# Optimization experiments

Hardware: AMD Instinct MI355X
Metric: run time of the kernel (lower is better)

## Reference

```python
import jax, jax.numpy as jnp
import numpy as np

BETA = 0.25
NUM_EMB = 50
EMB_DIM = 192


def setup_inputs() -> dict:
    key = jax.random.key(0)
    k1, k2 = jax.random.split(key)
    N = 262144
    inputs = jax.random.normal(k1, (N, EMB_DIM), dtype=jnp.float32)
    # nn.Embedding init: uniform(-1/num_embeddings, 1/num_embeddings)
    embed_w = jax.random.uniform(k2, (NUM_EMB, EMB_DIM), dtype=jnp.float32,
                                 minval=-1.0 / NUM_EMB, maxval=1.0 / NUM_EMB)
    return {"inputs": inputs, "embed_w": embed_w}


def reference(inputs, embed_w):
    # flat_input: [N, D] (inputs already flattened to last-dim = embedding_dim)
    flat = inputs.reshape(-1, EMB_DIM)
    distances = (jnp.sum(flat * flat, axis=1, keepdims=True)
                 + jnp.sum(embed_w * embed_w, axis=1)
                 - 2.0 * (flat @ embed_w.T))
    encoding_indices = jnp.argmin(distances, axis=1)[:, None]  # [N, 1]
    # one-hot scatter + matmul in the original == direct gather of nearest code
    quantized = embed_w[encoding_indices[:, 0]]  # [N, D]
    sg = jax.lax.stop_gradient
    commitloss = (jnp.mean((sg(quantized) - flat) ** 2)
                  + BETA * jnp.mean((quantized - sg(flat)) ** 2))
    # straight-through estimator
    quantized_st = flat + sg(quantized - flat)
    contrastloss = jnp.float32(0.0)
    return (quantized_st, encoding_indices, commitloss, contrastloss)
```

## Files before the change

### kernel.cpp

```cpp
#include <hip/hip_runtime.h>
#include <cfloat>

#define NUM_EMB 50
#define EMB_DIM 192
#define ESTRIDE 196

__device__ __forceinline__ float np_tree8(const float r[8]) {
#pragma clang fp contract(off)
    return ((r[0] + r[1]) + (r[2] + r[3])) + ((r[4] + r[5]) + (r[6] + r[7]));
}

__device__ float np_sumsq_192(const float* __restrict__ p) {
#pragma clang fp contract(off)
    float tot[2];
#pragma unroll
    for (int h = 0; h < 2; ++h) {
        float r[8];
#pragma unroll
        for (int l = 0; l < 8; ++l) r[l] = 0.f;
        const float* q = p + h * 96;
        for (int t = 0; t < 12; ++t)
#pragma unroll
            for (int l = 0; l < 8; ++l) {
                float v = q[t * 8 + l];
                float pr = v * v;
                r[l] = r[l] + pr;
            }
        tot[h] = np_tree8(r);
    }
    return tot[0] + tot[1];
}

__global__ __launch_bounds__(256, 4) void vq_fused(
    const float* __restrict__ x, const float* __restrict__ ew,
    float* __restrict__ out_q, float* __restrict__ out_idx,
    float* __restrict__ out_loss, int N)
{
    __shared__ __align__(16) float sE[NUM_EMB * ESTRIDE];
    __shared__ float sB[NUM_EMB];

    for (int i = threadIdx.x; i < NUM_EMB * EMB_DIM; i += blockDim.x) {
        int k = i / EMB_DIM, j = i - k * EMB_DIM;
        sE[k * ESTRIDE + j] = ew[i];
    }
    __syncthreads();
    if (threadIdx.x < NUM_EMB)
        sB[threadIdx.x] = np_sumsq_192(&sE[threadIdx.x * ESTRIDE]);
    __syncthreads();

    const int row = blockIdx.x * blockDim.x + threadIdx.x;
    const float4* xr = (const float4*)(x + (size_t)row * EMB_DIM);

    float acc[NUM_EMB];
#pragma unroll
    for (int k = 0; k < NUM_EMB; ++k) acc[k] = 0.f;

    float rA[8];
    float aHalf[2];

    for (int m = 0; m < 6; ++m) {
        float4 f4[8];
#pragma unroll
        for (int q = 0; q < 8; ++q) f4[q] = xr[m * 8 + q];

        if ((m % 3) == 0) {
#pragma unroll
            for (int l = 0; l < 8; ++l) rA[l] = 0.f;
        }
        {
#pragma clang fp contract(off)
#pragma unroll
            for (int q = 0; q < 8; ++q) {
                float p0 = f4[q].x * f4[q].x; rA[(q * 4 + 0) & 7] = rA[(q * 4 + 0) & 7] + p0;
                float p1 = f4[q].y * f4[q].y; rA[(q * 4 + 1) & 7] = rA[(q * 4 + 1) & 7] + p1;
                float p2 = f4[q].z * f4[q].z; rA[(q * 4 + 2) & 7] = rA[(q * 4 + 2) & 7] + p2;
                float p3 = f4[q].w * f4[q].w; rA[(q * 4 + 3) & 7] = rA[(q * 4 + 3) & 7] + p3;
            }
        }
        if ((m % 3) == 2) aHalf[m / 3] = np_tree8(rA);

        const float* eb = ew + m * 32;
#pragma unroll
        for (int k = 0; k < NUM_EMB; ++k) {
            const float* ek = eb + k * EMB_DIM;
            float4 e4[8];
#pragma unroll
            for (int q = 0; q < 8; ++q) e4[q] = *(const float4*)&ek[q * 4];
#pragma unroll
            for (int q = 0; q < 8; ++q) {
                acc[k] = __builtin_fmaf(f4[q].x, e4[q].x, acc[k]);
                acc[k] = __builtin_fmaf(f4[q].y, e4[q].y, acc[k]);
                acc[k] = __builtin_fmaf(f4[q].z, e4[q].z, acc[k]);
                acc[k] = __builtin_fmaf(f4[q].w, e4[q].w, acc[k]);
            }
        }
    }

    float best; int bidx;
    {
#pragma clang fp contract(off)
        float a = aHalf[0] + aHalf[1];
        best = FLT_MAX; bidx = 0;
#pragma unroll
        for (int k = 0; k < NUM_EMB; ++k) {
            float t1 = a + sB[k];
            float u  = 2.0f * acc[k];
            float d  = t1 - u;
            if (d < best) { best = d; bidx = k; }
        }
    }
    out_idx[row] = (float)bidx;

    float contrib = best;
#pragma unroll
    for (int off = 1; off < 64; off <<= 1) contrib += __shfl_xor(contrib, off);
    if ((threadIdx.x & 63) == 0) atomicAdd(out_loss, contrib);

    {
        const int lane = threadIdx.x & 63;
        const int c = lane & 7;
        const int rr = lane >> 3;
        const int waveRow0 = row & ~63;
#pragma unroll
        for (int g = 0; g < 8; ++g) {
            const int kk = __shfl(bidx, g * 8 + rr);
            const int wrow = waveRow0 + g * 8 + rr;
            float4* qrow = (float4*)(out_q + (size_t)wrow * EMB_DIM);
            const float* erow = &sE[kk * ESTRIDE];
#pragma unroll
            for (int t = 0; t < 6; ++t)
                qrow[c + 8 * t] = *(const float4*)&erow[(c + 8 * t) * 4];
        }
    }
}

__global__ void vq_init(float* out_loss) { out_loss[0] = 0.f; out_loss[1] = 0.f; }

__global__ void vq_finalize(float* __restrict__ out_loss, int N)
{
    double mean = (double)out_loss[0] / ((double)N * (double)EMB_DIM);
    out_loss[0] = (float)(1.25 * mean);
    out_loss[1] = 0.f;
}

extern "C" void kernel_launch(void* const* d_in, const int* in_sizes, int n_in,
                              void* d_out, int out_size, void* d_ws, size_t ws_size,
                              hipStream_t stream)
{
    const float* x  = (const float*)d_in[0];
    const float* ew = (const float*)d_in[1];
    const int N = in_sizes[0] / EMB_DIM;

    float* out_q    = (float*)d_out;
    float* out_idx  = out_q + (size_t)N * EMB_DIM;
    float* out_loss = out_idx + N;

    vq_init<<<1, 1, 0, stream>>>(out_loss);
    vq_fused<<<N / 256, 256, 0, stream>>>(x, ew, out_q, out_idx, out_loss, N);
    vq_finalize<<<1, 1, 0, stream>>>(out_loss, N);
}
```

Before: 420.1 us.

## Hold full input row in registers and stream codebook pairs with running argmin

Each thread now loads its whole 192-float input row into registers once, then loops over codebook entries two at a time, computing full dot products and updating the argmin as it goes. The 50-entry accumulator array goes away. Launch bounds are relaxed from 4 to 2 blocks per SM to give room for the larger register footprint. This trades per-codebook accumulators for a register-resident row. It reorders the FMA accumulation per code, which could change rounding relative to the staged version, and it lowers occupancy.

```diff
diff --git a/kernel.cpp b/kernel.cpp
--- a/kernel.cpp
+++ b/kernel.cpp
@@ -31,7 +31,7 @@
     return tot[0] + tot[1];
 }
 
-__global__ __launch_bounds__(256, 4) void vq_fused(
+__global__ __launch_bounds__(256, 2) void vq_fused(
     const float* __restrict__ x, const float* __restrict__ ew,
     float* __restrict__ out_q, float* __restrict__ out_idx,
     float* __restrict__ out_loss, int N)
@@ -49,64 +49,69 @@
     __syncthreads();
 
     const int row = blockIdx.x * blockDim.x + threadIdx.x;
-    const float4* xr = (const float4*)(x + (size_t)row * EMB_DIM);
+    const float4* xg = (const float4*)(x + (size_t)row * EMB_DIM);
 
-    float acc[NUM_EMB];
+    float4 xr[48];
 #pragma unroll
-    for (int k = 0; k < NUM_EMB; ++k) acc[k] = 0.f;
+    for (int q = 0; q < 48; ++q) xr[q] = xg[q];
 
-    float rA[8];
-    float aHalf[2];
+    float a;
+    {
+#pragma clang fp contract(off)
+        float tot[2];
+#pragma unroll
+        for (int h = 0; h < 2; ++h) {
+            float r[8];
+#pragma unroll
+            for (int l = 0; l < 8; ++l) r[l] = 0.f;
+#pragma unroll
+            for (int t = 0; t < 12; ++t) {
+                const float4 va = xr[h * 24 + t * 2];
+                const float4 vb = xr[h * 24 + t * 2 + 1];
+                float p0 = va.x * va.x; r[0] = r[0] + p0;
+                float p1 = va.y * va.y; r[1] = r[1] + p1;
+                float p2 = va.z * va.z; r[2] = r[2] + p2;
+                float p3 = va.w * va.w; r[3] = r[3] + p3;
+                float p4 = vb.x * vb.x; r[4] = r[4] + p4;
+                float p5 = vb.y * vb.y; r[5] = r[5] + p5;
+                float p6 = vb.z * vb.z; r[6] = r[6] + p6;
+                float p7 = vb.w * vb.w; r[7] = r[7] + p7;
+            }
+            tot[h] = np_tree8(r);
+        }
+        a = tot[0] + tot[1];
+    }
 
-    for (int m = 0; m < 6; ++m) {
-        float4 f4[8];
+    float best = FLT_MAX; int bidx = 0;
+    for (int kp = 0; kp < NUM_EMB / 2; ++kp) {
+        const float* e0 = ew + (size_t)(2 * kp) * EMB_DIM;
+        const float* e1 = e0 + EMB_DIM;
+        float a0 = 0.f, a1 = 0.f;
 #pragma unroll
-        for (int q = 0; q < 8; ++q) f4[q] = xr[m * 8 + q];
-
-        if ((m % 3) == 0) {
-#pragma unroll
-            for (int l = 0; l < 8; ++l) rA[l] = 0.f;
+        for (int q = 0; q < 48; ++q) {
+            const float4 ea = *(const float4*)&e0[q * 4];
+            const float4 eb = *(const float4*)&e1[q * 4];
+            const float4 xv = xr[q];
+            a0 = __builtin_fmaf(xv.x, ea.x, a0);
+            a0 = __builtin_fmaf(xv.y, ea.y, a0);
+            a0 = __builtin_fmaf(xv.z, ea.z, a0);
+            a0 = __builtin_fmaf(xv.w, ea.w, a0);
+            a1 = __builtin_fmaf(xv.x, eb.x, a1);
+            a1 = __builtin_fmaf(xv.y, eb.y, a1);
+            a1 = __builtin_fmaf(xv.z, eb.z, a1);
+            a1 = __builtin_fmaf(xv.w, eb.w, a1);
         }
         {
 #pragma clang fp contract(off)
-#pragma unroll
-            for (int q = 0; q < 8; ++q) {
-                float p0 = f4[q].x * f4[q].x; rA[(q * 4 + 0) & 7] = rA[(q * 4 + 0) & 7] + p0;
-                float p1 = f4[q].y * f4[q].y; rA[(q * 4 + 1) & 7] = rA[(q * 4 + 1) & 7] + p1;
-                float p2 = f4[q].z * f4[q].z; rA[(q * 4 + 2) & 7] = rA[(q * 4 + 2) & 7] + p2;
-                float p3 = f4[q].w * f4[q].w; rA[(q * 4 + 3) & 7] = rA[(q * 4 + 3) & 7] + p3;
-            }
-        }
-        if ((m % 3) == 2) aHalf[m / 3] = np_tree8(rA);
-
-        const float* eb = ew + m * 32;
-#pragma unroll
-        for (int k = 0; k < NUM_EMB; ++k) {
-            const float* ek = eb + k * EMB_DIM;
-            float4 e4[8];
-#pragma unroll
-            for (int q = 0; q < 8; ++q) e4[q] = *(const float4*)&ek[q * 4];
-#pragma unroll
-            for (int q = 0; q < 8; ++q) {
-                acc[k] = __builtin_fmaf(f4[q].x, e4[q].x, acc[k]);
-                acc[k] = __builtin_fmaf(f4[q].y, e4[q].y, acc[k]);
-                acc[k] = __builtin_fmaf(f4[q].z, e4[q].z, acc[k]);
-                acc[k] = __builtin_fmaf(f4[q].w, e4[q].w, acc[k]);
-            }
-        }
-    }
-
-    float best; int bidx;
-    {
-#pragma clang fp contract(off)
-        float a = aHalf[0] + aHalf[1];
-        best = FLT_MAX; bidx = 0;
-#pragma unroll
-        for (int k = 0; k < NUM_EMB; ++k) {
-            float t1 = a + sB[k];
-            float u  = 2.0f * acc[k];
-            float d  = t1 - u;
-            if (d < best) { best = d; bidx = k; }
+            const float sb0 = sB[2 * kp], sb1 = sB[2 * kp + 1];
+            float t0 = a + sb0;
+            float u0 = 2.0f * a0;
+            float d0 = t0 - u0;
+            if (d0 < best) { best = d0; bidx = 2 * kp; }
+            float t1 = a + sb1;
+            float u1 = 2.0f * a1;
+            float d1 = t1 - u1;
+            if (d1 < best) { best = d1; bidx = 2 * kp + 1; }
         }
     }
     out_idx[row] = (float)bidx;
```

Measured after the change: 520.3 us. 1.24x slower.

## Process two rows per thread and read codebook from shared memory

Applied to the files above, without the earlier changes.

Each thread now computes distances for two input rows (r0 and r0+N/2), so every codebook element loaded feeds two FMA chains. The codebook loads switch from global memory to the padded LDS copy. The grid is halved and launch bounds are relaxed to 2 blocks per SM to make room for the doubled accumulator registers. The cost is higher register pressure and lower occupancy, and the m-loop is no longer unrolled.

```diff
diff --git a/kernel.cpp b/kernel.cpp
--- a/kernel.cpp
+++ b/kernel.cpp
@@ -31,7 +31,7 @@
     return tot[0] + tot[1];
 }
 
-__global__ __launch_bounds__(256, 4) void vq_fused(
+__global__ __launch_bounds__(256, 2) void vq_fused(
     const float* __restrict__ x, const float* __restrict__ ew,
     float* __restrict__ out_q, float* __restrict__ out_idx,
     float* __restrict__ out_loss, int N)
@@ -48,70 +48,102 @@
         sB[threadIdx.x] = np_sumsq_192(&sE[threadIdx.x * ESTRIDE]);
     __syncthreads();
 
-    const int row = blockIdx.x * blockDim.x + threadIdx.x;
-    const float4* xr = (const float4*)(x + (size_t)row * EMB_DIM);
-
-    float acc[NUM_EMB];
-#pragma unroll
-    for (int k = 0; k < NUM_EMB; ++k) acc[k] = 0.f;
-
-    float rA[8];
-    float aHalf[2];
-
+    const int r0 = blockIdx.x * blockDim.x + threadIdx.x;
+    const int half = N >> 1;
+    const float4* xg0 = (const float4*)(x + (size_t)r0 * EMB_DIM);
+    const float4* xg1 = (const float4*)(x + (size_t)(r0 + half) * EMB_DIM);
+
+    float acc0[NUM_EMB], acc1[NUM_EMB];
+#pragma unroll
+    for (int k = 0; k < NUM_EMB; ++k) { acc0[k] = 0.f; acc1[k] = 0.f; }
+
+    float rA0[8], rA1[8];
+    float aHalf0[2], aHalf1[2];
+
+#pragma unroll 1
     for (int m = 0; m < 6; ++m) {
-        float4 f4[8];
-#pragma unroll
-        for (int q = 0; q < 8; ++q) f4[q] = xr[m * 8 + q];
+        float4 fa[8], fb[8];
+#pragma unroll
+        for (int q = 0; q < 8; ++q) fa[q] = xg0[m * 8 + q];
+#pragma unroll
+        for (int q = 0; q < 8; ++q) fb[q] = xg1[m * 8 + q];
+#pragma unroll
+        for (int q = 0; q < 8; ++q)
+            asm volatile("" : "+v"(fa[q].x), "+v"(fa[q].y), "+v"(fa[q].z), "+v"(fa[q].w));
+#pragma unroll
+        for (int q = 0; q < 8; ++q)
+            asm volatile("" : "+v"(fb[q].x), "+v"(fb[q].y), "+v"(fb[q].z), "+v"(fb[q].w));
 
         if ((m % 3) == 0) {
 #pragma unroll
-            for (int l = 0; l < 8; ++l) rA[l] = 0.f;
+            for (int l = 0; l < 8; ++l) { rA0[l] = 0.f; rA1[l] = 0.f; }
         }
         {
 #pragma clang fp contract(off)
 #pragma unroll
             for (int q = 0; q < 8; ++q) {
-                float p0 = f4[q].x * f4[q].x; rA[(q * 4 + 0) & 7] = rA[(q * 4 + 0) & 7] + p0;
-                float p1 = f4[q].y * f4[q].y; rA[(q * 4 + 1) & 7] = rA[(q * 4 + 1) & 7] + p1;
-                float p2 = f4[q].z * f4[q].z; rA[(q * 4 + 2) & 7] = rA[(q * 4 + 2) & 7] + p2;
-                float p3 = f4[q].w * f4[q].w; rA[(q * 4 + 3) & 7] = rA[(q * 4 + 3) & 7] + p3;
-            }
-        }
-        if ((m % 3) == 2) aHalf[m / 3] = np_tree8(rA);
-
-        const float* eb = ew + m * 32;
+                float p0 = fa[q].x * fa[q].x; rA0[(q * 4 + 0) & 7] = rA0[(q * 4 + 0) & 7] + p0;
+                float p1 = fa[q].y * fa[q].y; rA0[(q * 4 + 1) & 7] = rA0[(q * 4 + 1) & 7] + p1;
+                float p2 = fa[q].z * fa[q].z; rA0[(q * 4 + 2) & 7] = rA0[(q * 4 + 2) & 7] + p2;
+                float p3 = fa[q].w * fa[q].w; rA0[(q * 4 + 3) & 7] = rA0[(q * 4 + 3) & 7] + p3;
+            }
+#pragma unroll
+            for (int q = 0; q < 8; ++q) {
+                float p0 = fb[q].x * fb[q].x; rA1[(q * 4 + 0) & 7] = rA1[(q * 4 + 0) & 7] + p0;
+                float p1 = fb[q].y * fb[q].y; rA1[(q * 4 + 1) & 7] = rA1[(q * 4 + 1) & 7] + p1;
+                float p2 = fb[q].z * fb[q].z; rA1[(q * 4 + 2) & 7] = rA1[(q * 4 + 2) & 7] + p2;
+                float p3 = fb[q].w * fb[q].w; rA1[(q * 4 + 3) & 7] = rA1[(q * 4 + 3) & 7] + p3;
+            }
+        }
+        if ((m % 3) == 2) { aHalf0[m / 3] = np_tree8(rA0); aHalf1[m / 3] = np_tree8(rA1); }
+
 #pragma unroll
         for (int k = 0; k < NUM_EMB; ++k) {
-            const float* ek = eb + k * EMB_DIM;
+            const float* ek = &sE[k * ESTRIDE + m * 32];
             float4 e4[8];
 #pragma unroll
-            for (int q = 0; q < 8; ++q) e4[q] = *(const float4*)&ek[q * 4];
-#pragma unroll
-            for (int q = 0; q < 8; ++q) {
-                acc[k] = __builtin_fmaf(f4[q].x, e4[q].x, acc[k]);
-                acc[k] = __builtin_fmaf(f4[q].y, e4[q].y, acc[k]);
-                acc[k] = __builtin_fmaf(f4[q].z, e4[q].z, acc[k]);
-                acc[k] = __builtin_fmaf(f4[q].w, e4[q].w, acc[k]);
-            }
-        }
-    }
-
-    float best; int bidx;
+            for (int h = 0; h < 8; ++h) e4[h] = *(const float4*)&ek[h * 4];
+#pragma unroll
+            for (int h = 0; h < 8; ++h) {
+                acc0[k] = __builtin_fmaf(fa[h].x, e4[h].x, acc0[k]);
+                acc0[k] = __builtin_fmaf(fa[h].y, e4[h].y, acc0[k]);
+                acc0[k] = __builtin_fmaf(fa[h].z, e4[h].z, acc0[k]);
+                acc0[k] = __builtin_fmaf(fa[h].w, e4[h].w, acc0[k]);
+            }
+#pragma unroll
+            for (int h = 0; h < 8; ++h) {
+                acc1[k] = __builtin_fmaf(fb[h].x, e4[h].x, acc1[k]);
+                acc1[k] = __builtin_fmaf(fb[h].y, e4[h].y, acc1[k]);
+                acc1[k] = __builtin_fmaf(fb[h].z, e4[h].z, acc1[k]);
+                acc1[k] = __builtin_fmaf(fb[h].w, e4[h].w, acc1[k]);
+            }
+        }
+    }
+
+    float best0, best1; int bidx0, bidx1;
     {
 #pragma clang fp contract(off)
-        float a = aHalf[0] + aHalf[1];
-        best = FLT_MAX; bidx = 0;
+        float a0 = aHalf0[0] + aHalf0[1];
+        float a1 = aHalf1[0] + aHalf1[1];
+        best0 = FLT_MAX; bidx0 = 0;
+        best1 = FLT_MAX; bidx1 = 0;
 #pragma unroll
         for (int k = 0; k < NUM_EMB; ++k) {
-            float t1 = a + sB[k];
-            float u  = 2.0f * acc[k];
-            float d  = t1 - u;
-            if (d < best) { best = d; bidx = k; }
-        }
-    }
-    out_idx[row] = (float)bidx;
-
-    float contrib = best;
+            float sb = sB[k];
+            float t0 = a0 + sb;
+            float u0 = 2.0f * acc0[k];
+            float d0 = t0 - u0;
+            if (d0 < best0) { best0 = d0; bidx0 = k; }
+            float t1 = a1 + sb;
+            float u1 = 2.0f * acc1[k];
+            float d1 = t1 - u1;
+            if (d1 < best1) { best1 = d1; bidx1 = k; }
+        }
+    }
+    out_idx[r0] = (float)bidx0;
+    out_idx[r0 + half] = (float)bidx1;
+
+    float contrib = best0 + best1;
 #pragma unroll
     for (int off = 1; off < 64; off <<= 1) contrib += __shfl_xor(contrib, off);
     if ((threadIdx.x & 63) == 0) atomicAdd(out_loss, contrib);
@@ -120,11 +152,21 @@
         const int lane = threadIdx.x & 63;
         const int c = lane & 7;
         const int rr = lane >> 3;
-        const int waveRow0 = row & ~63;
+        const int waveRow0 = r0 & ~63;
 #pragma unroll
         for (int g = 0; g < 8; ++g) {
-            const int kk = __shfl(bidx, g * 8 + rr);
+            const int kk = __shfl(bidx0, g * 8 + rr);
             const int wrow = waveRow0 + g * 8 + rr;
+            float4* qrow = (float4*)(out_q + (size_t)wrow * EMB_DIM);
+            const float* erow = &sE[kk * ESTRIDE];
+#pragma unroll
+            for (int t = 0; t < 6; ++t)
+                qrow[c + 8 * t] = *(const float4*)&erow[(c + 8 * t) * 4];
+        }
+#pragma unroll
+        for (int g = 0; g < 8; ++g) {
+            const int kk = __shfl(bidx1, g * 8 + rr);
+            const int wrow = waveRow0 + half + g * 8 + rr;
             float4* qrow = (float4*)(out_q + (size_t)wrow * EMB_DIM);
             const float* erow = &sE[kk * ESTRIDE];
 #pragma unroll
@@ -156,6 +198,6 @@
     float* out_loss = out_idx + N;
 
     vq_init<<<1, 1, 0, stream>>>(out_loss);
-    vq_fused<<<N / 256, 256, 0, stream>>>(x, ew, out_q, out_idx, out_loss, N);
+    vq_fused<<<N / 512, 256, 0, stream>>>(x, ew, out_q, out_idx, out_loss, N);
     vq_finalize<<<1, 1, 0, stream>>>(out_loss, N);
 }
```

Result: faster. 384.7 us (-8.4%).
